# Kernel optimization log

Measured on AMD Instinct MI355X. Metric: run time of the kernel, lower is better.

## Reference

```python
import jax, jax.numpy as jnp
import numpy as np

B, S, D = 4, 2048, 512      # batch, seq_len, input_dim
E, H = 512, 8               # embed_dim, n_heads
HD = E // H                 # head_dim
ALPHA = 1.0                 # LRSA temperature


def setup_inputs() -> dict:
    key = jax.random.key(0)
    kx, kw1, kw2 = jax.random.split(key, 3)
    # xavier_uniform bounds for the two Linear layers (bias init is 0, as in module)
    b_qkv = float(np.sqrt(6.0 / (D + 3 * E)))
    b_o = float(np.sqrt(6.0 / (E + E)))
    return {
        "x": jax.random.normal(kx, (B, S, D), dtype=jnp.float32),
        "Wqkv": jax.random.uniform(kw1, (3 * E, D), jnp.float32, -b_qkv, b_qkv),
        "bqkv": jnp.zeros((3 * E,), jnp.float32),
        "Wo": jax.random.uniform(kw2, (E, E), jnp.float32, -b_o, b_o),
        "bo": jnp.zeros((E,), jnp.float32),
    }


def reference(x, Wqkv, bqkv, Wo, bo):
    Bx, Sx, _ = x.shape
    # QKV projection: [B,S,3E] -> [B,S,H,3*HD] -> [B,H,S,3*HD]
    qkv = (x @ Wqkv.T + bqkv).reshape(Bx, Sx, H, 3 * HD).transpose(0, 2, 1, 3)
    q, k, v = jnp.split(qkv, 3, axis=-1)  # each [B,H,S,HD]

    # LRSA: pairwise squared L2 distance logits ||q_i - k_j||^2
    q_norm2 = jnp.sum(q * q, axis=-1, keepdims=True)        # [B,H,S,1]
    k_norm2 = jnp.sum(k * k, axis=-1)[..., None, :]         # [B,H,1,S]
    qk = jnp.einsum("bhqd,bhkd->bhqk", q, k)                # [B,H,S,S]
    logits = q_norm2 - 2.0 * qk + k_norm2

    # global normalizers: frobenius norm of q, max per-token L2 norm of x
    fro_q = jnp.sqrt(jnp.sum(q * q))
    inf_2_x = jnp.max(jnp.sqrt(jnp.sum(x * x, axis=-1)))
    logits = logits / fro_q / inf_2_x

    attention = jax.nn.softmax(-ALPHA * logits, axis=-1)    # [B,H,S,S]
    values = jnp.einsum("bhqk,bhkd->bhqd", attention, v)    # [B,H,S,HD]
    values = values.transpose(0, 2, 1, 3).reshape(Bx, Sx, E)
    return values @ Wo.T + bo
```

## Files before the change

kernel.cpp:

```cpp
#include <hip/hip_runtime.h>
#include <hip/hip_bf16.h>
#include <math.h>

#define B_ 4
#define S_ 2048
#define D_ 512
#define E_ 512
#define H_ 8
#define HD_ 64
#define ALPHA_ 1.0f
#define M_ (B_*S_)
#define LOG2E_ 1.44269504088896340736f

typedef __attribute__((ext_vector_type(8))) short bf16x8;
typedef __attribute__((ext_vector_type(4))) float f32x4;

__device__ inline unsigned short f2bf(float f) {
    union { __hip_bfloat16 h; unsigned short u; } cv;
    cv.h = __float2bfloat16(f);
    return cv.u;
}
__device__ inline unsigned pack2bf(float a, float b) {
    union { __hip_bfloat162 h; unsigned u; } cv;
    cv.h = __float22bfloat162_rn(make_float2(a, b));
    return cv.u;
}
__device__ inline void gload16(const void* g, void* l) {
    __builtin_amdgcn_global_load_lds(
        (const __attribute__((address_space(1))) unsigned int*)g,
        (__attribute__((address_space(3))) unsigned int*)l, 16, 0, 0);
}
__device__ inline void gload4(const void* g, void* l) {
    __builtin_amdgcn_global_load_lds(
        (const __attribute__((address_space(1))) unsigned int*)g,
        (__attribute__((address_space(3))) unsigned int*)l, 4, 0, 0);
}

__global__ __launch_bounds__(256) void prep(const float* __restrict__ x,
                                            const float* __restrict__ Wqkv,
                                            const float* __restrict__ Wo,
                                            unsigned short* __restrict__ xbf,
                                            unsigned short* __restrict__ Wqkvb,
                                            unsigned short* __restrict__ Wob,
                                            float* __restrict__ xmax) {
    const int t   = threadIdx.x;
    const int bid = blockIdx.x;
    if (bid < 2048) {
        __shared__ float red[4];
        const int wid = t >> 6, lane = t & 63;
        const int row = bid * 4 + wid;
        const float* xr = &x[(size_t)row * D_ + lane * 8];
        const float4 a = *(const float4*)xr;
        const float4 b = *(const float4*)(xr + 4);
        float ss = a.x*a.x + a.y*a.y + a.z*a.z + a.w*a.w
                 + b.x*b.x + b.y*b.y + b.z*b.z + b.w*b.w;
        uint4 o;
        o.x = pack2bf(a.x, a.y); o.y = pack2bf(a.z, a.w);
        o.z = pack2bf(b.x, b.y); o.w = pack2bf(b.z, b.w);
        *(uint4*)&xbf[(size_t)row * D_ + lane * 8] = o;
        #pragma unroll
        for (int off = 32; off; off >>= 1) ss += __shfl_xor(ss, off);
        if (lane == 0) red[wid] = ss;
        __syncthreads();
        if (t == 0)
            xmax[bid] = fmaxf(fmaxf(red[0], red[1]), fmaxf(red[2], red[3]));
    } else {
        const int i  = (bid - 2048) * 256 + t;
        const int nq = 3 * E_ * D_ / 8;
        const float* src; unsigned short* dst; int j;
        if (i < nq) { src = Wqkv; dst = Wqkvb; j = i; }
        else        { src = Wo;   dst = Wob;   j = i - nq; }
        const float4 a = *(const float4*)&src[(size_t)j * 8];
        const float4 b = *(const float4*)&src[(size_t)j * 8 + 4];
        uint4 o;
        o.x = pack2bf(a.x, a.y); o.y = pack2bf(a.z, a.w);
        o.z = pack2bf(b.x, b.y); o.w = pack2bf(b.z, b.w);
        *(uint4*)&dst[(size_t)j * 8] = o;
    }
}

template<int N, int MODE>
__global__ __launch_bounds__(256) void gemm_mfma(const unsigned short* __restrict__ Abf,
                                                 const unsigned short* __restrict__ Wbf,
                                                 const float* __restrict__ bias,
                                                 void* __restrict__ out0,
                                                 void* __restrict__ out1,
                                                 void* __restrict__ out2,
                                                 float* __restrict__ part,
                                                 float* __restrict__ kn2) {
    __shared__ __align__(16) char At[16384];
    __shared__ __align__(16) char Wt[16384];

    const int t  = threadIdx.x;
    const int w  = t >> 6;
    const int l  = t & 63;
    const int g  = l >> 4;
    const int c  = l & 15;
    const int wm = w >> 1;
    const int wn = w & 1;
    const int m0 = blockIdx.y * 128;
    const int n0 = blockIdx.x * 128;

    f32x4 acc[4][4];
    #pragma unroll
    for (int i = 0; i < 4; ++i)
        #pragma unroll
        for (int j = 0; j < 4; ++j)
            #pragma unroll
            for (int r = 0; r < 4; ++r) acc[i][j][r] = 0.f;

    const int lr3 = l >> 3;
    const int colSwz = ((l & 7) * 16) ^ (lr3 << 4);
    const char* pA = (const char*)Abf + (size_t)(m0 + w * 8 + lr3) * 1024 + colSwz;
    const char* pB = (const char*)Wbf + (size_t)(n0 + w * 8 + lr3) * 1024 + colSwz;
    char* lA = At + w * 1024;
    char* lB = Wt + w * 1024;

    for (int k0 = 0; k0 < 512; k0 += 64) {
        __syncthreads();
        #pragma unroll
        for (int j = 0; j < 4; ++j) {
            gload16(pA + (size_t)j * 32768 + k0 * 2, lA + j * 4096);
            gload16(pB + (size_t)j * 32768 + k0 * 2, lB + j * 4096);
        }
        __syncthreads();

        bf16x8 af[4][2], wf[4][2];
        #pragma unroll
        for (int mt = 0; mt < 4; ++mt) {
            const int row = wm * 64 + mt * 16 + c;
            const int sw  = (row & 7) << 4;
            #pragma unroll
            for (int kc = 0; kc < 2; ++kc)
                af[mt][kc] = *(const bf16x8*)(At + row * 128 + (((kc * 4 + g) * 16) ^ sw));
        }
        #pragma unroll
        for (int nt = 0; nt < 4; ++nt) {
            const int row = wn * 64 + nt * 16 + c;
            const int sw  = (row & 7) << 4;
            #pragma unroll
            for (int kc = 0; kc < 2; ++kc)
                wf[nt][kc] = *(const bf16x8*)(Wt + row * 128 + (((kc * 4 + g) * 16) ^ sw));
        }
        #pragma unroll
        for (int mt = 0; mt < 4; ++mt)
            #pragma unroll
            for (int nt = 0; nt < 4; ++nt) {
                acc[mt][nt] = __builtin_amdgcn_mfma_f32_16x16x32_bf16(af[mt][0], wf[nt][0], acc[mt][nt], 0, 0, 0);
                acc[mt][nt] = __builtin_amdgcn_mfma_f32_16x16x32_bf16(af[mt][1], wf[nt][1], acc[mt][nt], 0, 0, 0);
            }
    }

    if (MODE == 1) {
        #pragma unroll
        for (int mt = 0; mt < 4; ++mt)
            #pragma unroll
            for (int reg = 0; reg < 4; ++reg) {
                const int m = m0 + wm * 64 + mt * 16 + g * 4 + reg;
                #pragma unroll
                for (int nt = 0; nt < 4; ++nt) {
                    const int n = n0 + wn * 64 + nt * 16 + c;
                    ((float*)out0)[(size_t)m * N + n] = acc[mt][nt][reg] + bias[n];
                }
            }
        return;
    }

    const int hb  = 2 * blockIdx.x + wn;
    const int cls = hb % 3;
    const int h   = hb / 3;
    const int b   = m0 >> 11;
    const int s0w = (m0 & 2047) + wm * 64;
    const size_t bhS = ((size_t)b * H_ + h) * S_;

    float kp[4][4];
    #pragma unroll
    for (int i = 0; i < 4; ++i)
        #pragma unroll
        for (int j = 0; j < 4; ++j) kp[i][j] = 0.f;

    if (cls == 2) {
        unsigned short* Vt_ = (unsigned short*)out2;
        #pragma unroll
        for (int nt = 0; nt < 4; ++nt) {
            const int n = n0 + wn * 64 + nt * 16 + c;
            const float bv = bias[n];
            const int d = nt * 16 + c;
            unsigned short* dbase = Vt_ + (((size_t)b * H_ + h) * HD_ + d) * S_ + s0w;
            #pragma unroll
            for (int mt = 0; mt < 4; ++mt) {
                uint2 pk;
                pk.x = pack2bf(acc[mt][nt][0] + bv, acc[mt][nt][1] + bv);
                pk.y = pack2bf(acc[mt][nt][2] + bv, acc[mt][nt][3] + bv);
                *(uint2*)&dbase[mt * 16 + g * 4] = pk;
            }
        }
    } else {
        unsigned short* dst0 = (cls == 0) ? (unsigned short*)out0 : (unsigned short*)out1;
        #pragma unroll
        for (int nt = 0; nt < 4; ++nt) {
            const int n = n0 + wn * 64 + nt * 16 + c;
            const float bv = bias[n];
            const int d = nt * 16 + c;
            #pragma unroll
            for (int mt = 0; mt < 4; ++mt)
                #pragma unroll
                for (int reg = 0; reg < 4; ++reg) {
                    const int s = s0w + mt * 16 + g * 4 + reg;
                    const float val = acc[mt][nt][reg] + bv;
                    kp[mt][reg] = fmaf(val, val, kp[mt][reg]);
                    dst0[(bhS + s) * HD_ + d] = f2bf(val);
                }
        }
    }

    __syncthreads();
    if (cls == 1) {
        float* scratch = (float*)At + wm * 1088;
        #pragma unroll
        for (int i = 0; i < 16; ++i) scratch[l * 17 + i] = kp[i >> 2][i & 3];
        asm volatile("s_waitcnt lgkmcnt(0)" ::: "memory");
        __builtin_amdgcn_sched_barrier(0);
        float sum = 0.f;
        #pragma unroll
        for (int cc = 0; cc < 16; ++cc)
            sum += scratch[(g * 16 + cc) * 17 + c];
        const int s = s0w + (c >> 2) * 16 + g * 4 + (c & 3);
        kn2[bhS + s] = sum;
    }
    __syncthreads();

    float qss = 0.f;
    if (cls == 0) {
        #pragma unroll
        for (int i = 0; i < 4; ++i)
            #pragma unroll
            for (int j = 0; j < 4; ++j) qss += kp[i][j];
    }
    float* red = (float*)At;
    red[t] = qss;
    __syncthreads();
    for (int s = 128; s; s >>= 1) {
        if (t < s) red[t] += red[t + s];
        __syncthreads();
    }
    if (t == 0) part[blockIdx.y * gridDim.x + blockIdx.x] = red[0];
}

__global__ __launch_bounds__(256) void finalize_scale(const float* __restrict__ part,
                                                      const float* __restrict__ xmax,
                                                      float* __restrict__ scal) {
    __shared__ float rs[256], rm[256];
    const int t = threadIdx.x;
    float ss = 0.f, mx = 0.f;
    for (int i = t; i < 768; i += 256) ss += part[i];
    for (int i = t; i < 2048; i += 256) mx = fmaxf(mx, xmax[i]);
    rs[t] = ss; rm[t] = mx;
    __syncthreads();
    for (int s = 128; s; s >>= 1) {
        if (t < s) { rs[t] += rs[t + s]; rm[t] = fmaxf(rm[t], rm[t + s]); }
        __syncthreads();
    }
    if (t == 0) scal[0] = ALPHA_ * LOG2E_ / (sqrtf(rs[0]) * sqrtf(rm[0]));
}

__global__ __launch_bounds__(512, 2) void attn_mfma(const unsigned short* __restrict__ Qb,
                                                    const unsigned short* __restrict__ Kb,
                                                    const unsigned short* __restrict__ Vtb,
                                                    const float* __restrict__ KN2,
                                                    const float* __restrict__ scal,
                                                    unsigned short* __restrict__ VALS) {
    __shared__ __align__(16) char lds[49664];
    char* Kl = lds;
    char* Vl = lds + 16384;
    char* Pl = lds + 32768;
    char* knl = lds + 49152;

    const int t  = threadIdx.x;
    const int w  = t >> 6;
    const int l  = t & 63;
    const int g  = l >> 4;
    const int c  = l & 15;
    const int bid  = blockIdx.y * gridDim.x + blockIdx.x;
    const int swid = (bid & 7) * 64 + (bid >> 3);
    const int bh = swid >> 4;
    const int qb = swid & 15;
    const float sc    = scal[0];
    const float ts2   = 2.0f * sc;
    const float nscal = -sc;

    const int qrow = qb * 128 + w * 16 + c;
    const size_t qoff = ((size_t)bh * S_ + qrow) * HD_;
    const bf16x8 qf0 = *(const bf16x8*)&Qb[qoff + g * 8];
    const bf16x8 qf1 = *(const bf16x8*)&Qb[qoff + 32 + g * 8];

    f32x4 acc[4];
    #pragma unroll
    for (int dt = 0; dt < 4; ++dt)
        #pragma unroll
        for (int r = 0; r < 4; ++r) acc[dt][r] = 0.f;
    float lpart = 0.f;

    const float* kn2g = &KN2[(size_t)bh * S_];
    char* Pw = Pl + w * 2048;
    const int swc = (c & 7) << 4;

    int offF[4][2];
    #pragma unroll
    for (int i = 0; i < 4; ++i) {
        offF[i][0] = (i * 16 + c) * 128 + ((g * 16) ^ swc);
        offF[i][1] = (i * 16 + c) * 128 + ((64 + g * 16) ^ swc);
    }
    int offPW[4];
    #pragma unroll
    for (int kt = 0; kt < 4; ++kt)
        offPW[kt] = c * 128 + ((kt * 32 + g * 8) ^ swc);
    const int offPA0 = c * 128 + ((g * 16) ^ swc);
    const int offPA1 = c * 128 + ((64 + g * 16) ^ swc);

    const int lr3 = l >> 3;
    const int colSwz = ((l & 7) * 16) ^ (lr3 << 4);
    const char* pK = (const char*)Kb + ((size_t)bh * S_ * HD_) * 2
                   + (size_t)(w * 8 + lr3) * 128 + colSwz;
    const char* pV = (const char*)Vtb + ((size_t)bh * HD_ * S_) * 2
                   + (size_t)(w * 8 + lr3) * (S_ * 2) + colSwz;
    char* lK = Kl + w * 1024;
    char* lV = Vl + w * 1024;

#define STAGE(T, buf) do {                                                    \
        gload16(pK + (size_t)(T) * 8192, lK + (buf) * 8192);                  \
        gload16(pV + (size_t)(T) * 128,  lV + (buf) * 8192);                  \
        if (w == 0) gload4(kn2g + (T) * 64 + l, knl + (buf) * 256);           \
    } while (0)

    auto compute_tile = [&](int cur) {
        const char* Kc = Kl + cur * 8192;
        const char* Vc = Vl + cur * 8192;
        const float* knc = (const float*)(knl + cur * 256);
        float sl[16];
        #pragma unroll
        for (int kt = 0; kt < 4; ++kt) {
            const bf16x8 ka0 = *(const bf16x8*)(Kc + offF[kt][0]);
            const bf16x8 ka1 = *(const bf16x8*)(Kc + offF[kt][1]);
            f32x4 sacc = {0.f, 0.f, 0.f, 0.f};
            sacc = __builtin_amdgcn_mfma_f32_16x16x32_bf16(ka0, qf0, sacc, 0, 0, 0);
            sacc = __builtin_amdgcn_mfma_f32_16x16x32_bf16(ka1, qf1, sacc, 0, 0, 0);
            const f32x4 kn4 = *(const f32x4*)&knc[kt * 16 + g * 4];
            #pragma unroll
            for (int rg = 0; rg < 4; ++rg)
                sl[kt * 4 + rg] = fmaf(sacc[rg], ts2, nscal * kn4[rg]);
        }

        float p[16];
        #pragma unroll
        for (int j = 0; j < 16; ++j) { p[j] = exp2f(sl[j]); lpart += p[j]; }

        #pragma unroll
        for (int kt = 0; kt < 4; ++kt) {
            uint2 pk;
            pk.x = pack2bf(p[kt * 4 + 0], p[kt * 4 + 1]);
            pk.y = pack2bf(p[kt * 4 + 2], p[kt * 4 + 3]);
            *(uint2*)(Pw + offPW[kt]) = pk;
        }
        asm volatile("s_waitcnt lgkmcnt(0)" ::: "memory");
        __builtin_amdgcn_sched_barrier(0);

        const bf16x8 pa0 = *(const bf16x8*)(Pw + offPA0);
        const bf16x8 pa1 = *(const bf16x8*)(Pw + offPA1);
        #pragma unroll
        for (int dt = 0; dt < 4; ++dt) {
            const bf16x8 vb0 = *(const bf16x8*)(Vc + offF[dt][0]);
            const bf16x8 vb1 = *(const bf16x8*)(Vc + offF[dt][1]);
            acc[dt] = __builtin_amdgcn_mfma_f32_16x16x32_bf16(pa0, vb0, acc[dt], 0, 0, 0);
            acc[dt] = __builtin_amdgcn_mfma_f32_16x16x32_bf16(pa1, vb1, acc[dt], 0, 0, 0);
        }
    };

    STAGE(0, 0);
    __syncthreads();
    for (int T = 0; T < 32; ++T) {
        const int cur = T & 1;
        if (T < 31) STAGE(T + 1, cur ^ 1);
        compute_tile(cur);
        __syncthreads();
    }
#undef STAGE

    lpart += __shfl_xor(lpart, 16);
    lpart += __shfl_xor(lpart, 32);

    const int b = bh >> 3, h = bh & 7;
    #pragma unroll
    for (int reg = 0; reg < 4; ++reg) {
        const float lq  = __shfl(lpart, g * 4 + reg);
        const float inv = 1.0f / lq;
        const int qg = qb * 128 + w * 16 + g * 4 + reg;
        unsigned short* dst = &VALS[((size_t)b * S_ + qg) * E_ + h * HD_];
        #pragma unroll
        for (int dt = 0; dt < 4; ++dt)
            dst[dt * 16 + c] = f2bf(acc[dt][reg] * inv);
    }
}

extern "C" void kernel_launch(void* const* d_in, const int* in_sizes, int n_in,
                              void* d_out, int out_size, void* d_ws, size_t ws_size,
                              hipStream_t stream) {
    const float* x    = (const float*)d_in[0];
    const float* Wqkv = (const float*)d_in[1];
    const float* bqkv = (const float*)d_in[2];
    const float* Wo   = (const float*)d_in[3];
    const float* bo   = (const float*)d_in[4];
    float* out = (float*)d_out;

    char* ws = (char*)d_ws;
    unsigned short* Qb    = (unsigned short*)(ws);
    unsigned short* Kb    = (unsigned short*)(ws + ((size_t) 8 << 20));
    unsigned short* Vtb   = (unsigned short*)(ws + ((size_t)16 << 20));
    unsigned short* VALb  = (unsigned short*)(ws + ((size_t)24 << 20));
    unsigned short* xbf   = (unsigned short*)(ws + ((size_t)32 << 20));
    unsigned short* Wqkvb = (unsigned short*)(ws + ((size_t)40 << 20));
    unsigned short* Wob   = (unsigned short*)(ws + ((size_t)42 << 20));
    float* KN2  = (float*)(ws + ((size_t)43 << 20));
    float* PART = (float*)(ws + ((size_t)43 << 20) + (256 << 10));
    float* XMAX = (float*)(ws + ((size_t)43 << 20) + (260 << 10));
    float* SCAL = (float*)(ws + ((size_t)43 << 20) + (272 << 10));

    prep<<<2560, 256, 0, stream>>>(x, Wqkv, Wo, xbf, Wqkvb, Wob, XMAX);

    gemm_mfma<3 * E_, 0><<<dim3(12, 64), 256, 0, stream>>>(xbf, Wqkvb, bqkv, Qb, Kb, Vtb, PART, KN2);

    finalize_scale<<<1, 256, 0, stream>>>(PART, XMAX, SCAL);

    attn_mfma<<<dim3(16, 32), 512, 0, stream>>>(Qb, Kb, Vtb, KN2, SCAL, VALb);

    gemm_mfma<E_, 1><<<dim3(4, 64), 256, 0, stream>>>(VALb, Wob, bo, out, nullptr, nullptr, nullptr, nullptr);
}
```

Baseline: 116.2 us.

## Switch attention kernel to 32x32x16 MFMA with register-shuffled P operand

The attention kernel now uses 32x32x16 bf16 MFMA tiles, with each wave covering 32 query rows and 4 waves per block instead of 8 waves of 16 rows. The softmax probabilities are re-laid into the A-operand format through cross-half-wave shuffles instead of a round trip through LDS, so the P staging buffer and its wait/sync are removed. The larger tiles are meant to reduce LDS operand traffic per flop. The trade-off is more accumulator registers per thread and fewer waves per block, which may lower occupancy and latency hiding.

```diff
diff --git a/kernel.cpp b/kernel.cpp
--- a/kernel.cpp
+++ b/kernel.cpp
@@ -14,6 +14,7 @@
 
 typedef __attribute__((ext_vector_type(8))) short bf16x8;
 typedef __attribute__((ext_vector_type(4))) float f32x4;
+typedef __attribute__((ext_vector_type(16))) float f32x16;
 
 __device__ inline unsigned short f2bf(float f) {
     union { __hip_bfloat16 h; unsigned short u; } cv;
@@ -264,23 +265,22 @@
     if (t == 0) scal[0] = ALPHA_ * LOG2E_ / (sqrtf(rs[0]) * sqrtf(rm[0]));
 }
 
-__global__ __launch_bounds__(512, 2) void attn_mfma(const unsigned short* __restrict__ Qb,
+__global__ __launch_bounds__(256, 2) void attn_mfma(const unsigned short* __restrict__ Qb,
                                                     const unsigned short* __restrict__ Kb,
                                                     const unsigned short* __restrict__ Vtb,
                                                     const float* __restrict__ KN2,
                                                     const float* __restrict__ scal,
                                                     unsigned short* __restrict__ VALS) {
-    __shared__ __align__(16) char lds[49664];
-    char* Kl = lds;
-    char* Vl = lds + 16384;
-    char* Pl = lds + 32768;
-    char* knl = lds + 49152;
-
-    const int t  = threadIdx.x;
-    const int w  = t >> 6;
-    const int l  = t & 63;
-    const int g  = l >> 4;
-    const int c  = l & 15;
+    __shared__ __align__(16) char lds[33280];
+    char* Kl  = lds;
+    char* Vl  = lds + 16384;
+    char* knl = lds + 32768;
+
+    const int t   = threadIdx.x;
+    const int w   = t >> 6;
+    const int l   = t & 63;
+    const int h   = l >> 5;
+    const int c32 = l & 31;
     const int bid  = blockIdx.y * gridDim.x + blockIdx.x;
     const int swid = (bid & 7) * 64 + (bid >> 3);
     const int bh = swid >> 4;
@@ -289,47 +289,43 @@
     const float ts2   = 2.0f * sc;
     const float nscal = -sc;
 
-    const int qrow = qb * 128 + w * 16 + c;
+    const int qrow = qb * 128 + w * 32 + c32;
     const size_t qoff = ((size_t)bh * S_ + qrow) * HD_;
-    const bf16x8 qf0 = *(const bf16x8*)&Qb[qoff + g * 8];
-    const bf16x8 qf1 = *(const bf16x8*)&Qb[qoff + 32 + g * 8];
-
-    f32x4 acc[4];
-    #pragma unroll
-    for (int dt = 0; dt < 4; ++dt)
-        #pragma unroll
-        for (int r = 0; r < 4; ++r) acc[dt][r] = 0.f;
+    bf16x8 qf[4];
+    #pragma unroll
+    for (int dc = 0; dc < 4; ++dc)
+        qf[dc] = *(const bf16x8*)&Qb[qoff + dc * 16 + h * 8];
+
+    f32x16 oacc0, oacc1;
+    #pragma unroll
+    for (int i = 0; i < 16; ++i) { oacc0[i] = 0.f; oacc1[i] = 0.f; }
     float lpart = 0.f;
 
     const float* kn2g = &KN2[(size_t)bh * S_];
-    char* Pw = Pl + w * 2048;
-    const int swc = (c & 7) << 4;
-
-    int offF[4][2];
-    #pragma unroll
-    for (int i = 0; i < 4; ++i) {
-        offF[i][0] = (i * 16 + c) * 128 + ((g * 16) ^ swc);
-        offF[i][1] = (i * 16 + c) * 128 + ((64 + g * 16) ^ swc);
-    }
-    int offPW[4];
-    #pragma unroll
-    for (int kt = 0; kt < 4; ++kt)
-        offPW[kt] = c * 128 + ((kt * 32 + g * 8) ^ swc);
-    const int offPA0 = c * 128 + ((g * 16) ^ swc);
-    const int offPA1 = c * 128 + ((64 + g * 16) ^ swc);
+
+    const int swz = (l & 7) << 4;
+    int offF[2][4];
+    #pragma unroll
+    for (int a = 0; a < 2; ++a)
+        #pragma unroll
+        for (int x = 0; x < 4; ++x)
+            offF[a][x] = (a * 32 + c32) * 128 + ((x * 32 + h * 16) ^ swz);
 
     const int lr3 = l >> 3;
     const int colSwz = ((l & 7) * 16) ^ (lr3 << 4);
     const char* pK = (const char*)Kb + ((size_t)bh * S_ * HD_) * 2
-                   + (size_t)(w * 8 + lr3) * 128 + colSwz;
+                   + (size_t)(w * 16 + lr3) * 128 + colSwz;
     const char* pV = (const char*)Vtb + ((size_t)bh * HD_ * S_) * 2
-                   + (size_t)(w * 8 + lr3) * (S_ * 2) + colSwz;
-    char* lK = Kl + w * 1024;
-    char* lV = Vl + w * 1024;
+                   + (size_t)(w * 16 + lr3) * (S_ * 2) + colSwz;
+    char* lK = Kl + w * 2048;
+    char* lV = Vl + w * 2048;
 
 #define STAGE(T, buf) do {                                                    \
-        gload16(pK + (size_t)(T) * 8192, lK + (buf) * 8192);                  \
-        gload16(pV + (size_t)(T) * 128,  lV + (buf) * 8192);                  \
+        gload16(pK + (size_t)(T) * 8192,        lK + (buf) * 8192);           \
+        gload16(pK + (size_t)(T) * 8192 + 1024, lK + (buf) * 8192 + 1024);    \
+        gload16(pV + (size_t)(T) * 128,                   lV + (buf) * 8192); \
+        gload16(pV + (size_t)(T) * 128 + (size_t)8 * S_ * 2,                  \
+                lV + (buf) * 8192 + 1024);                                    \
         if (w == 0) gload4(kn2g + (T) * 64 + l, knl + (buf) * 256);           \
     } while (0)
 
@@ -337,42 +333,53 @@
         const char* Kc = Kl + cur * 8192;
         const char* Vc = Vl + cur * 8192;
         const float* knc = (const float*)(knl + cur * 256);
-        float sl[16];
-        #pragma unroll
-        for (int kt = 0; kt < 4; ++kt) {
-            const bf16x8 ka0 = *(const bf16x8*)(Kc + offF[kt][0]);
-            const bf16x8 ka1 = *(const bf16x8*)(Kc + offF[kt][1]);
-            f32x4 sacc = {0.f, 0.f, 0.f, 0.f};
-            sacc = __builtin_amdgcn_mfma_f32_16x16x32_bf16(ka0, qf0, sacc, 0, 0, 0);
-            sacc = __builtin_amdgcn_mfma_f32_16x16x32_bf16(ka1, qf1, sacc, 0, 0, 0);
-            const f32x4 kn4 = *(const f32x4*)&knc[kt * 16 + g * 4];
-            #pragma unroll
-            for (int rg = 0; rg < 4; ++rg)
-                sl[kt * 4 + rg] = fmaf(sacc[rg], ts2, nscal * kn4[rg]);
-        }
-
-        float p[16];
-        #pragma unroll
-        for (int j = 0; j < 16; ++j) { p[j] = exp2f(sl[j]); lpart += p[j]; }
-
-        #pragma unroll
-        for (int kt = 0; kt < 4; ++kt) {
-            uint2 pk;
-            pk.x = pack2bf(p[kt * 4 + 0], p[kt * 4 + 1]);
-            pk.y = pack2bf(p[kt * 4 + 2], p[kt * 4 + 3]);
-            *(uint2*)(Pw + offPW[kt]) = pk;
-        }
-        asm volatile("s_waitcnt lgkmcnt(0)" ::: "memory");
-        __builtin_amdgcn_sched_barrier(0);
-
-        const bf16x8 pa0 = *(const bf16x8*)(Pw + offPA0);
-        const bf16x8 pa1 = *(const bf16x8*)(Pw + offPA1);
-        #pragma unroll
-        for (int dt = 0; dt < 4; ++dt) {
-            const bf16x8 vb0 = *(const bf16x8*)(Vc + offF[dt][0]);
-            const bf16x8 vb1 = *(const bf16x8*)(Vc + offF[dt][1]);
-            acc[dt] = __builtin_amdgcn_mfma_f32_16x16x32_bf16(pa0, vb0, acc[dt], 0, 0, 0);
-            acc[dt] = __builtin_amdgcn_mfma_f32_16x16x32_bf16(pa1, vb1, acc[dt], 0, 0, 0);
+
+        unsigned ownw[8][2];
+        #pragma unroll
+        for (int st = 0; st < 2; ++st) {
+            f32x16 sacc;
+            #pragma unroll
+            for (int i = 0; i < 16; ++i) sacc[i] = 0.f;
+            #pragma unroll
+            for (int dc = 0; dc < 4; ++dc) {
+                const bf16x8 ka = *(const bf16x8*)(Kc + offF[st][dc]);
+                sacc = __builtin_amdgcn_mfma_f32_32x32x16_bf16(ka, qf[dc], sacc, 0, 0, 0);
+            }
+            #pragma unroll
+            for (int r4 = 0; r4 < 4; ++r4) {
+                const f32x4 kn4 = *(const f32x4*)&knc[st * 32 + 8 * r4 + 4 * h];
+                float pv[4];
+                #pragma unroll
+                for (int m = 0; m < 4; ++m) {
+                    const float sl = fmaf(sacc[4 * r4 + m], ts2, nscal * kn4[m]);
+                    pv[m] = exp2f(sl);
+                    lpart += pv[m];
+                }
+                ownw[st * 4 + r4][0] = pack2bf(pv[0], pv[1]);
+                ownw[st * 4 + r4][1] = pack2bf(pv[2], pv[3]);
+            }
+        }
+
+        unsigned rcv[4][2];
+        #pragma unroll
+        for (int s = 0; s < 4; ++s) {
+            const unsigned s0 = h ? ownw[2 * s][0] : ownw[2 * s + 1][0];
+            const unsigned s1 = h ? ownw[2 * s][1] : ownw[2 * s + 1][1];
+            rcv[s][0] = __shfl_xor(s0, 32);
+            rcv[s][1] = __shfl_xor(s1, 32);
+        }
+
+        #pragma unroll
+        for (int kc = 0; kc < 4; ++kc) {
+            union { bf16x8 v; unsigned u[4]; } fr;
+            fr.u[0] = h ? rcv[kc][0] : ownw[2 * kc][0];
+            fr.u[1] = h ? rcv[kc][1] : ownw[2 * kc][1];
+            fr.u[2] = h ? ownw[2 * kc + 1][0] : rcv[kc][0];
+            fr.u[3] = h ? ownw[2 * kc + 1][1] : rcv[kc][1];
+            const bf16x8 vb0 = *(const bf16x8*)(Vc + offF[0][kc]);
+            const bf16x8 vb1 = *(const bf16x8*)(Vc + offF[1][kc]);
+            oacc0 = __builtin_amdgcn_mfma_f32_32x32x16_bf16(fr.v, vb0, oacc0, 0, 0, 0);
+            oacc1 = __builtin_amdgcn_mfma_f32_32x32x16_bf16(fr.v, vb1, oacc1, 0, 0, 0);
         }
     };
 
@@ -386,19 +393,18 @@
     }
 #undef STAGE
 
-    lpart += __shfl_xor(lpart, 16);
     lpart += __shfl_xor(lpart, 32);
 
-    const int b = bh >> 3, h = bh & 7;
-    #pragma unroll
-    for (int reg = 0; reg < 4; ++reg) {
-        const float lq  = __shfl(lpart, g * 4 + reg);
+    const int b = bh >> 3, head = bh & 7;
+    #pragma unroll
+    for (int reg = 0; reg < 16; ++reg) {
+        const int q_local = (reg & 3) + 8 * (reg >> 2) + 4 * h;
+        const float lq  = __shfl(lpart, q_local);
         const float inv = 1.0f / lq;
-        const int qg = qb * 128 + w * 16 + g * 4 + reg;
-        unsigned short* dst = &VALS[((size_t)b * S_ + qg) * E_ + h * HD_];
-        #pragma unroll
-        for (int dt = 0; dt < 4; ++dt)
-            dst[dt * 16 + c] = f2bf(acc[dt][reg] * inv);
+        const int s = qb * 128 + w * 32 + q_local;
+        unsigned short* dst = &VALS[((size_t)b * S_ + s) * E_ + head * HD_];
+        dst[c32]      = f2bf(oacc0[reg] * inv);
+        dst[32 + c32] = f2bf(oacc1[reg] * inv);
     }
 }
 
@@ -431,7 +437,7 @@
 
     finalize_scale<<<1, 256, 0, stream>>>(PART, XMAX, SCAL);
 
-    attn_mfma<<<dim3(16, 32), 512, 0, stream>>>(Qb, Kb, Vtb, KN2, SCAL, VALb);
+    attn_mfma<<<dim3(16, 32), 256, 0, stream>>>(Qb, Kb, Vtb, KN2, SCAL, VALb);
 
     gemm_mfma<E_, 1><<<dim3(4, 64), 256, 0, stream>>>(VALb, Wob, bo, out, nullptr, nullptr, nullptr, nullptr);
 }
```

Result: slower. 122.6 us (+5.5%).

## Double-buffer GEMM LDS tiles, raise MFMA priority, use native exp2 in attention

Applied to the files above, without the earlier changes.

The projection GEMM now keeps two LDS buffers for the A and W tiles and issues the global-to-LDS loads for the next k-step before computing the current one. This needs only one barrier per iteration and lets load latency overlap with the MFMA work. The MFMA block is wrapped in s_setprio to favour matrix issue. In the attention kernel, exp2f is replaced by the hardware exp2 builtin to skip denormal and range handling. The cost is doubled GEMM LDS (64KB), which may reduce occupancy, and a slightly different exp2 precision.

```diff
diff --git a/kernel.cpp b/kernel.cpp
--- a/kernel.cpp
+++ b/kernel.cpp
@@ -88,8 +88,8 @@
                                                  void* __restrict__ out2,
                                                  float* __restrict__ part,
                                                  float* __restrict__ kn2) {
-    __shared__ __align__(16) char At[16384];
-    __shared__ __align__(16) char Wt[16384];
+    __shared__ __align__(16) char At[2][16384];
+    __shared__ __align__(16) char Wt[2][16384];
 
     const int t  = threadIdx.x;
     const int w  = t >> 6;
@@ -113,17 +113,20 @@
     const int colSwz = ((l & 7) * 16) ^ (lr3 << 4);
     const char* pA = (const char*)Abf + (size_t)(m0 + w * 8 + lr3) * 1024 + colSwz;
     const char* pB = (const char*)Wbf + (size_t)(n0 + w * 8 + lr3) * 1024 + colSwz;
-    char* lA = At + w * 1024;
-    char* lB = Wt + w * 1024;
-
-    for (int k0 = 0; k0 < 512; k0 += 64) {
-        __syncthreads();
+
+    auto gstage = [&](int k0, int buf) {
         #pragma unroll
         for (int j = 0; j < 4; ++j) {
-            gload16(pA + (size_t)j * 32768 + k0 * 2, lA + j * 4096);
-            gload16(pB + (size_t)j * 32768 + k0 * 2, lB + j * 4096);
-        }
-        __syncthreads();
+            gload16(pA + (size_t)j * 32768 + (size_t)k0 * 2, At[buf] + w * 1024 + j * 4096);
+            gload16(pB + (size_t)j * 32768 + (size_t)k0 * 2, Wt[buf] + w * 1024 + j * 4096);
+        }
+    };
+
+    gstage(0, 0);
+    __syncthreads();
+    for (int i = 0; i < 8; ++i) {
+        const int buf = i & 1;
+        if (i < 7) gstage((i + 1) * 64, buf ^ 1);
 
         bf16x8 af[4][2], wf[4][2];
         #pragma unroll
@@ -132,7 +135,7 @@
             const int sw  = (row & 7) << 4;
             #pragma unroll
             for (int kc = 0; kc < 2; ++kc)
-                af[mt][kc] = *(const bf16x8*)(At + row * 128 + (((kc * 4 + g) * 16) ^ sw));
+                af[mt][kc] = *(const bf16x8*)(At[buf] + row * 128 + (((kc * 4 + g) * 16) ^ sw));
         }
         #pragma unroll
         for (int nt = 0; nt < 4; ++nt) {
@@ -140,8 +143,9 @@
             const int sw  = (row & 7) << 4;
             #pragma unroll
             for (int kc = 0; kc < 2; ++kc)
-                wf[nt][kc] = *(const bf16x8*)(Wt + row * 128 + (((kc * 4 + g) * 16) ^ sw));
-        }
+                wf[nt][kc] = *(const bf16x8*)(Wt[buf] + row * 128 + (((kc * 4 + g) * 16) ^ sw));
+        }
+        __builtin_amdgcn_s_setprio(1);
         #pragma unroll
         for (int mt = 0; mt < 4; ++mt)
             #pragma unroll
@@ -149,6 +153,8 @@
                 acc[mt][nt] = __builtin_amdgcn_mfma_f32_16x16x32_bf16(af[mt][0], wf[nt][0], acc[mt][nt], 0, 0, 0);
                 acc[mt][nt] = __builtin_amdgcn_mfma_f32_16x16x32_bf16(af[mt][1], wf[nt][1], acc[mt][nt], 0, 0, 0);
             }
+        __builtin_amdgcn_s_setprio(0);
+        __syncthreads();
     }
 
     if (MODE == 1) {
@@ -216,7 +222,7 @@
 
     __syncthreads();
     if (cls == 1) {
-        float* scratch = (float*)At + wm * 1088;
+        float* scratch = (float*)&At[0][0] + wm * 1088;
         #pragma unroll
         for (int i = 0; i < 16; ++i) scratch[l * 17 + i] = kp[i >> 2][i & 3];
         asm volatile("s_waitcnt lgkmcnt(0)" ::: "memory");
@@ -237,7 +243,7 @@
             #pragma unroll
             for (int j = 0; j < 4; ++j) qss += kp[i][j];
     }
-    float* red = (float*)At;
+    float* red = (float*)&At[0][0];
     red[t] = qss;
     __syncthreads();
     for (int s = 128; s; s >>= 1) {
@@ -268,7 +274,7 @@
                                                     const unsigned short* __restrict__ Kb,
                                                     const unsigned short* __restrict__ Vtb,
                                                     const float* __restrict__ KN2,
-                                                    const float* __restrict__ scal,
+                                                    const float* __restrict__ SCAL,
                                                     unsigned short* __restrict__ VALS) {
     __shared__ __align__(16) char lds[49664];
     char* Kl = lds;
@@ -285,7 +291,8 @@
     const int swid = (bid & 7) * 64 + (bid >> 3);
     const int bh = swid >> 4;
     const int qb = swid & 15;
-    const float sc    = scal[0];
+
+    const float sc    = SCAL[0];
     const float ts2   = 2.0f * sc;
     const float nscal = -sc;
 
@@ -353,7 +360,10 @@
 
         float p[16];
         #pragma unroll
-        for (int j = 0; j < 16; ++j) { p[j] = exp2f(sl[j]); lpart += p[j]; }
+        for (int j = 0; j < 16; ++j) {
+            p[j] = __builtin_amdgcn_exp2f(sl[j]);
+            lpart += p[j];
+        }
 
         #pragma unroll
         for (int kt = 0; kt < 4; ++kt) {
```

Result: faster. 102.3 us (median of 3 runs) (-11.9%).
